# Performance work log

Hardware: AMD Instinct MI355X
Metric: run time of the kernel (lower is better)

The kernel has to match this reference:

```python
import jax, jax.numpy as jnp
import numpy as np

BLOCK = 4096  # bitsandbytes blockwise-quantization block size


def setup_inputs() -> dict:
    key = jax.random.key(0)
    k_x, k_w, k_a, k_c, k_b = jax.random.split(key, 5)
    out_features, in_features = 16384, 4096
    numel = out_features * in_features
    x = jax.random.normal(k_x, (2, 2048, in_features), dtype=jnp.float32)
    # int8 codes stored as indices into the 256-entry dequant table
    qweight = jax.random.randint(k_w, (out_features, in_features), 0, 256, dtype=jnp.int32)
    absmax = jax.random.uniform(k_a, (numel // BLOCK,), dtype=jnp.float32)
    code = jax.random.normal(k_c, (256,), dtype=jnp.float32)
    bias = jax.random.normal(k_b, (out_features,), dtype=jnp.float32)
    return {"x": x, "qweight": qweight, "absmax": absmax, "code": code, "bias": bias}


def reference(x, qweight, absmax, code, bias):
    # dequantize_blockwise: w[i] = code[q[i]] * absmax[i // BLOCK]
    out_f, in_f = qweight.shape
    w = (code[qweight.reshape(-1)].reshape(-1, BLOCK) * absmax[:, None]).reshape(out_f, in_f)
    # F.linear(x, W, b) = x @ W^T + b
    return jnp.einsum("bsi,oi->bso", x, w) + bias
```

## Files before the change

kernel.cpp:

```cpp
#include <hip/hip_runtime.h>
#include <hip/hip_bf16.h>


typedef __bf16 bf16x8 __attribute__((ext_vector_type(8)));
typedef __bf16 bf16x4 __attribute__((ext_vector_type(4)));
typedef float  f32x4  __attribute__((ext_vector_type(4)));

#define GLD_LDS(gp, lp) \
    __builtin_amdgcn_global_load_lds((const __attribute__((address_space(1))) void*)(gp), \
                                     (__attribute__((address_space(3))) void*)(lp), 16, 0, 0)

static constexpr int M = 4096;
static constexpr int N = 16384;
static constexpr int K = 4096;
static constexpr int BM = 128;
static constexpr int BN = 128;
static constexpr int BK = 32;

__global__ __launch_bounds__(256) void dequant_w(const int4* __restrict__ q4,
                                                 const float* __restrict__ code,
                                                 const float* __restrict__ absmax,
                                                 bf16x4* __restrict__ W)
{
    unsigned gid = blockIdx.x * 256u + threadIdx.x;
    int4 qv = q4[gid];
    float am = absmax[gid >> 10];
    bf16x4 w;
    w[0] = (__bf16)(code[qv.x] * am);
    w[1] = (__bf16)(code[qv.y] * am);
    w[2] = (__bf16)(code[qv.z] * am);
    w[3] = (__bf16)(code[qv.w] * am);
    W[gid] = w;
}

__global__ __launch_bounds__(256) void cvt_x(const float4* __restrict__ x,
                                             bf16x4* __restrict__ xb)
{
    unsigned gid = blockIdx.x * 256u + threadIdx.x;
    float4 v = x[gid];
    bf16x4 o;
    o[0] = (__bf16)v.x;
    o[1] = (__bf16)v.y;
    o[2] = (__bf16)v.z;
    o[3] = (__bf16)v.w;
    xb[gid] = o;
}

__global__ __launch_bounds__(256) void gemm_bt_bias(const __bf16* __restrict__ A,
                                                    const __bf16* __restrict__ B,
                                                    const float* __restrict__ bias,
                                                    float* __restrict__ C)
{
    __shared__ __bf16 As[BM * BK];
    __shared__ __bf16 Bs[BN * BK];

    const int tid  = threadIdx.x;
    const int lane = tid & 63;
    const int wave = tid >> 6;
    const int bm = blockIdx.y * BM;
    const int bn = blockIdx.x * BN;
    const int wm = (wave >> 1) * 64;
    const int wn = (wave & 1) * 64;

    const int srow = tid >> 2;
    const int skcol = (tid & 3) * 8;

    const __bf16* ag0 = A + (long long)(bm + srow) * K + skcol;
    const __bf16* bg0 = B + (long long)(bn + srow) * K + skcol;

    f32x4 acc[4][4] = {};

    const int fr = lane & 15;
    const int fk = (lane >> 4) * 8;

    for (int k0 = 0; k0 < K; k0 += BK) {
        __syncthreads();
        GLD_LDS(ag0 + k0,            As + tid * 8);
        GLD_LDS(ag0 + k0 + 64 * K,   As + 2048 + tid * 8);
        GLD_LDS(bg0 + k0,            Bs + tid * 8);
        GLD_LDS(bg0 + k0 + 64 * K,   Bs + 2048 + tid * 8);
        __syncthreads();

        bf16x8 af[4], bfr[4];
#pragma unroll
        for (int i = 0; i < 4; ++i)
            af[i] = *(const bf16x8*)(As + (wm + i * 16 + fr) * BK + fk);
#pragma unroll
        for (int i = 0; i < 4; ++i)
            bfr[i] = *(const bf16x8*)(Bs + (wn + i * 16 + fr) * BK + fk);

#pragma unroll
        for (int mi = 0; mi < 4; ++mi)
#pragma unroll
            for (int ni = 0; ni < 4; ++ni)
                acc[mi][ni] = __builtin_amdgcn_mfma_f32_16x16x32_bf16(
                    af[mi], bfr[ni], acc[mi][ni], 0, 0, 0);
    }

    const int cn = lane & 15;
    const int rq = (lane >> 4) * 4;
#pragma unroll
    for (int ni = 0; ni < 4; ++ni) {
        const int n = bn + wn + ni * 16 + cn;
        const float bv = bias[n];
#pragma unroll
        for (int mi = 0; mi < 4; ++mi) {
#pragma unroll
            for (int r = 0; r < 4; ++r) {
                const int m = bm + wm + mi * 16 + rq + r;
                C[(long long)m * N + n] = acc[mi][ni][r] + bv;
            }
        }
    }
}

extern "C" void kernel_launch(void* const* d_in, const int* in_sizes, int n_in,
                              void* d_out, int out_size, void* d_ws, size_t ws_size,
                              hipStream_t stream)
{
    const float* x      = (const float*)d_in[0];
    const int*   qw     = (const int*)d_in[1];
    const float* absmax = (const float*)d_in[2];
    const float* code   = (const float*)d_in[3];
    const float* bias   = (const float*)d_in[4];
    float* out = (float*)d_out;

    __bf16* Wb = (__bf16*)d_ws;
    __bf16* Xb = (__bf16*)((char*)d_ws + (size_t)N * K * sizeof(__bf16));

    dequant_w<<<(N * (long long)K) / 4 / 256, 256, 0, stream>>>(
        (const int4*)qw, code, absmax, (bf16x4*)Wb);

    cvt_x<<<(M * (long long)K) / 4 / 256, 256, 0, stream>>>(
        (const float4*)x, (bf16x4*)Xb);

    dim3 grid(N / BN, M / BM);
    gemm_bt_bias<<<grid, 256, 0, stream>>>(Xb, Wb, bias, out);
}
```

Measured before the change: 1.114 ms.

## Rework bf16 GEMM into 256x256 double-buffered swizzled-LDS pipeline with tile remap

```diff
diff --git a/kernel.cpp b/kernel.cpp
--- a/kernel.cpp
+++ b/kernel.cpp
@@ -13,23 +13,28 @@
 static constexpr int M = 4096;
 static constexpr int N = 16384;
 static constexpr int K = 4096;
-static constexpr int BM = 128;
-static constexpr int BN = 128;
-static constexpr int BK = 32;
+static constexpr int BM = 256;
+static constexpr int BN = 256;
+static constexpr int BK = 64;
+static constexpr int NT = K / BK;
+static constexpr int LDS_BYTES = 2 * 2 * 256 * BK * 2;
 
 __global__ __launch_bounds__(256) void dequant_w(const int4* __restrict__ q4,
                                                  const float* __restrict__ code,
                                                  const float* __restrict__ absmax,
                                                  bf16x4* __restrict__ W)
 {
+    __shared__ float lc[256];
+    lc[threadIdx.x] = code[threadIdx.x];
+    __syncthreads();
     unsigned gid = blockIdx.x * 256u + threadIdx.x;
     int4 qv = q4[gid];
     float am = absmax[gid >> 10];
     bf16x4 w;
-    w[0] = (__bf16)(code[qv.x] * am);
-    w[1] = (__bf16)(code[qv.y] * am);
-    w[2] = (__bf16)(code[qv.z] * am);
-    w[3] = (__bf16)(code[qv.w] * am);
+    w[0] = (__bf16)(lc[qv.x] * am);
+    w[1] = (__bf16)(lc[qv.y] * am);
+    w[2] = (__bf16)(lc[qv.z] * am);
+    w[3] = (__bf16)(lc[qv.w] * am);
     W[gid] = w;
 }
 
@@ -46,69 +51,137 @@
     xb[gid] = o;
 }
 
-__global__ __launch_bounds__(256) void gemm_bt_bias(const __bf16* __restrict__ A,
-                                                    const __bf16* __restrict__ B,
-                                                    const float* __restrict__ bias,
-                                                    float* __restrict__ C)
-{
-    __shared__ __bf16 As[BM * BK];
-    __shared__ __bf16 Bs[BN * BK];
-
+
+__device__ __forceinline__ void stage_half(const __bf16* gp, char* ldsbase, int h, int tid)
+{
+    GLD_LDS(gp + (size_t)(h * 128) * K,      ldsbase + h * 16384 +        tid * 16);
+    GLD_LDS(gp + (size_t)(h * 128 + 64) * K, ldsbase + h * 16384 + 8192 + tid * 16);
+}
+
+__device__ __forceinline__ void tile_step(const __bf16*& agn, const __bf16*& bgn,
+                                          const char* cA, const char* cB,
+                                          char* nA, char* nB, bool pf, int tid,
+                                          int baseA, int baseB, f32x4 (&acc)[8][4])
+{
+    if (pf) {
+        stage_half(agn, nA, 0, tid);
+        stage_half(agn, nA, 1, tid);
+        stage_half(bgn, nB, 0, tid);
+        asm volatile("s_waitcnt vmcnt(6)" ::: "memory");
+    } else {
+        asm volatile("s_waitcnt vmcnt(0)" ::: "memory");
+    }
+    __builtin_amdgcn_s_barrier();
+
+    if (pf) {
+        stage_half(bgn, nB, 1, tid);
+        agn += BK;
+        bgn += BK;
+    }
+
+    bf16x8 bfr[4][2], af[2][2];
+#pragma unroll
+    for (int ni = 0; ni < 4; ++ni) {
+        bfr[ni][0] = *(const bf16x8*)(cB + (baseB + ni * 2048));
+        bfr[ni][1] = *(const bf16x8*)(cB + ((baseB + ni * 2048) ^ 64));
+    }
+    af[0][0] = *(const bf16x8*)(cA + baseA);
+    af[0][1] = *(const bf16x8*)(cA + (baseA ^ 64));
+    af[1][0] = *(const bf16x8*)(cA + (baseA + 2048));
+    af[1][1] = *(const bf16x8*)(cA + ((baseA + 2048) ^ 64));
+
+    __builtin_amdgcn_s_barrier();
+    __builtin_amdgcn_s_setprio(1);
+#pragma unroll
+    for (int kk = 0; kk < 2; ++kk)
+#pragma unroll
+        for (int i = 0; i < 2; ++i)
+#pragma unroll
+            for (int ni = 0; ni < 4; ++ni)
+                acc[i][ni] = __builtin_amdgcn_mfma_f32_16x16x32_bf16(
+                    af[i][kk], bfr[ni][kk], acc[i][ni], 0, 0, 0);
+    __builtin_amdgcn_s_setprio(0);
+    __builtin_amdgcn_s_barrier();
+
+#pragma unroll
+    for (int p = 1; p < 4; ++p) {
+        af[0][0] = *(const bf16x8*)(cA + (baseA + (2 * p) * 2048));
+        af[0][1] = *(const bf16x8*)(cA + ((baseA + (2 * p) * 2048) ^ 64));
+        af[1][0] = *(const bf16x8*)(cA + (baseA + (2 * p + 1) * 2048));
+        af[1][1] = *(const bf16x8*)(cA + ((baseA + (2 * p + 1) * 2048) ^ 64));
+        __builtin_amdgcn_s_barrier();
+        __builtin_amdgcn_s_setprio(1);
+#pragma unroll
+        for (int kk = 0; kk < 2; ++kk)
+#pragma unroll
+            for (int i = 0; i < 2; ++i)
+#pragma unroll
+                for (int ni = 0; ni < 4; ++ni)
+                    acc[2 * p + i][ni] = __builtin_amdgcn_mfma_f32_16x16x32_bf16(
+                        af[i][kk], bfr[ni][kk], acc[2 * p + i][ni], 0, 0, 0);
+        __builtin_amdgcn_s_setprio(0);
+        __builtin_amdgcn_s_barrier();
+    }
+}
+
+__global__ __launch_bounds__(512, 2) void gemm_bt_bias(const __bf16* __restrict__ A,
+                                                       const __bf16* __restrict__ B,
+                                                       const float* __restrict__ bias,
+                                                       float* __restrict__ C)
+{
+    extern __shared__ char lds[];
     const int tid  = threadIdx.x;
     const int lane = tid & 63;
     const int wave = tid >> 6;
-    const int bm = blockIdx.y * BM;
-    const int bn = blockIdx.x * BN;
-    const int wm = (wave >> 1) * 64;
-    const int wn = (wave & 1) * 64;
-
-    const int srow = tid >> 2;
-    const int skcol = (tid & 3) * 8;
-
-    const __bf16* ag0 = A + (long long)(bm + srow) * K + skcol;
-    const __bf16* bg0 = B + (long long)(bn + srow) * K + skcol;
-
-    f32x4 acc[4][4] = {};
-
-    const int fr = lane & 15;
-    const int fk = (lane >> 4) * 8;
-
-    for (int k0 = 0; k0 < K; k0 += BK) {
-        __syncthreads();
-        GLD_LDS(ag0 + k0,            As + tid * 8);
-        GLD_LDS(ag0 + k0 + 64 * K,   As + 2048 + tid * 8);
-        GLD_LDS(bg0 + k0,            Bs + tid * 8);
-        GLD_LDS(bg0 + k0 + 64 * K,   Bs + 2048 + tid * 8);
-        __syncthreads();
-
-        bf16x8 af[4], bfr[4];
-#pragma unroll
-        for (int i = 0; i < 4; ++i)
-            af[i] = *(const bf16x8*)(As + (wm + i * 16 + fr) * BK + fk);
-#pragma unroll
-        for (int i = 0; i < 4; ++i)
-            bfr[i] = *(const bf16x8*)(Bs + (wn + i * 16 + fr) * BK + fk);
-
-#pragma unroll
-        for (int mi = 0; mi < 4; ++mi)
-#pragma unroll
-            for (int ni = 0; ni < 4; ++ni)
-                acc[mi][ni] = __builtin_amdgcn_mfma_f32_16x16x32_bf16(
-                    af[mi], bfr[ni], acc[mi][ni], 0, 0, 0);
+    const int wm = wave >> 2;
+    const int wn = wave & 3;
+
+    const int cpx  = (int)gridDim.x >> 3;
+    const int flat = ((int)blockIdx.x & 7) * cpx + ((int)blockIdx.x >> 3);
+    const int bm = (flat & (M / BM - 1)) * BM;
+    const int bn = (flat / (M / BM)) * BN;
+
+    const int r0 = tid >> 3;
+    const int cs = (tid & 7) ^ (r0 & 7);
+    const __bf16* ag = A + (size_t)(bm + r0) * K + cs * 8;
+    const __bf16* bg = B + (size_t)(bn + r0) * K + cs * 8;
+
+    char* const ldsA0 = lds;
+    char* const ldsB0 = lds + 32768;
+    char* const ldsA1 = lds + 65536;
+    char* const ldsB1 = lds + 98304;
+
+    const int swz   = ((lane >> 4) ^ (lane & 7)) << 4;
+    const int baseA = (wm * 128 + (lane & 15)) * 128 + swz;
+    const int baseB = (wn * 64  + (lane & 15)) * 128 + swz;
+
+    f32x4 acc[8][4] = {};
+
+    stage_half(ag, ldsA0, 0, tid);
+    stage_half(ag, ldsA0, 1, tid);
+    stage_half(bg, ldsB0, 0, tid);
+    stage_half(bg, ldsB0, 1, tid);
+
+    const __bf16* agn = ag + BK;
+    const __bf16* bgn = bg + BK;
+
+    for (int t2 = 0; t2 < NT; t2 += 2) {
+        tile_step(agn, bgn, ldsA0, ldsB0, ldsA1, ldsB1, true,         tid, baseA, baseB, acc);
+        tile_step(agn, bgn, ldsA1, ldsB1, ldsA0, ldsB0, t2 + 2 < NT,  tid, baseA, baseB, acc);
     }
 
     const int cn = lane & 15;
     const int rq = (lane >> 4) * 4;
 #pragma unroll
     for (int ni = 0; ni < 4; ++ni) {
-        const int n = bn + wn + ni * 16 + cn;
+        const int n = bn + wn * 64 + ni * 16 + cn;
         const float bv = bias[n];
 #pragma unroll
-        for (int mi = 0; mi < 4; ++mi) {
+        for (int mi = 0; mi < 8; ++mi) {
 #pragma unroll
             for (int r = 0; r < 4; ++r) {
-                const int m = bm + wm + mi * 16 + rq + r;
-                C[(long long)m * N + n] = acc[mi][ni][r] + bv;
+                const int m = bm + wm * 128 + mi * 16 + rq + r;
+                C[(size_t)m * N + n] = acc[mi][ni][r] + bv;
             }
         }
     }
@@ -128,12 +201,19 @@
     __bf16* Wb = (__bf16*)d_ws;
     __bf16* Xb = (__bf16*)((char*)d_ws + (size_t)N * K * sizeof(__bf16));
 
+    static bool attr_set = false;
+    if (!attr_set) {
+        (void)hipFuncSetAttribute((const void*)gemm_bt_bias,
+                                  hipFuncAttributeMaxDynamicSharedMemorySize, LDS_BYTES);
+        attr_set = true;
+    }
+
     dequant_w<<<(N * (long long)K) / 4 / 256, 256, 0, stream>>>(
         (const int4*)qw, code, absmax, (bf16x4*)Wb);
 
     cvt_x<<<(M * (long long)K) / 4 / 256, 256, 0, stream>>>(
         (const float4*)x, (bf16x4*)Xb);
 
-    dim3 grid(N / BN, M / BM);
-    gemm_bt_bias<<<grid, 256, 0, stream>>>(Xb, Wb, bias, out);
-}
+    gemm_bt_bias<<<dim3((M / BM) * (N / BN)), dim3(512), LDS_BYTES, stream>>>(
+        Xb, Wb, bias, out);
+}
```

Result: faster. 1.006 ms (-9.7%).
